# Kernel optimization log

Measured on AMD Instinct MI355X. Metric: run time of the kernel, lower is better.

The kernel has to match this reference:

```python
import jax, jax.numpy as jnp
import numpy as np

EMB_DIM = 2048
N_HEADS = 32
N_KV_HEADS = 8
HEAD_DIM = EMB_DIM // N_HEADS  # 64
N_REP = N_HEADS // N_KV_HEADS  # 4
B = 1
T = 2048


def setup_inputs() -> dict:
    key = jax.random.key(0)
    ks = jax.random.split(key, 7)
    x = jax.random.normal(ks[0], (B, T, EMB_DIM), dtype=jnp.float32)
    # RoPE tables, standard: cos/sin of shape (T, head_dim)
    inv_freq = 1.0 / (10000.0 ** (np.arange(0, HEAD_DIM, 2, dtype=np.float32) / HEAD_DIM))
    pos = np.arange(T, dtype=np.float32)
    ang = pos[:, None] * inv_freq[None, :]            # (T, head_dim/2)
    ang = np.concatenate([ang, ang], axis=-1)         # (T, head_dim)
    cos = jnp.asarray(np.cos(ang), dtype=jnp.float32)
    sin = jnp.asarray(np.sin(ang), dtype=jnp.float32)
    s = 0.02
    Wq = jax.random.normal(ks[1], (EMB_DIM, EMB_DIM), dtype=jnp.float32) * s
    Wk = jax.random.normal(ks[2], (N_KV_HEADS * HEAD_DIM, EMB_DIM), dtype=jnp.float32) * s
    Wv = jax.random.normal(ks[3], (N_KV_HEADS * HEAD_DIM, EMB_DIM), dtype=jnp.float32) * s
    Wo = jax.random.normal(ks[4], (EMB_DIM, EMB_DIM), dtype=jnp.float32) * s
    return {"x": x, "cos": cos, "sin": sin, "Wq": Wq, "Wk": Wk, "Wv": Wv, "Wo": Wo}


def apply_rope(t, cos, sin):
    # t: (b, h, T, d); cos/sin: (T, d)
    d = t.shape[-1]
    x1, x2 = t[..., : d // 2], t[..., d // 2:]
    rotated = jnp.concatenate([-x2, x1], axis=-1)
    return t * cos[None, None] + rotated * sin[None, None]


def reference(x, cos, sin, Wq, Wk, Wv, Wo):
    b, n_tok, _ = x.shape
    q = (x @ Wq.T).reshape(b, n_tok, N_HEADS, HEAD_DIM).transpose(0, 2, 1, 3)
    k = (x @ Wk.T).reshape(b, n_tok, N_KV_HEADS, HEAD_DIM).transpose(0, 2, 1, 3)
    v = (x @ Wv.T).reshape(b, n_tok, N_KV_HEADS, HEAD_DIM).transpose(0, 2, 1, 3)
    q = apply_rope(q, cos, sin)
    k = apply_rope(k, cos, sin)
    # repeat_interleave KV heads to n_heads
    k = jnp.repeat(k, N_REP, axis=1)
    v = jnp.repeat(v, N_REP, axis=1)
    scores = jnp.einsum("bhqd,bhkd->bhqk", q, k) / jnp.sqrt(jnp.float32(HEAD_DIM))
    causal = jnp.tril(jnp.ones((n_tok, n_tok), dtype=bool))
    scores = jnp.where(causal[None, None], scores, -jnp.inf)
    weights = jax.nn.softmax(scores, axis=-1)
    ctx = jnp.einsum("bhqk,bhkd->bhqd", weights, v)
    ctx = ctx.transpose(0, 2, 1, 3).reshape(b, n_tok, EMB_DIM)
    return ctx @ Wo.T
```

## Files before the change

kernel.cpp:

```cpp
#include <hip/hip_runtime.h>
#include <hip/hip_bf16.h>
#include <stdint.h>

#define EMB   2048
#define TOK   2048
#define NH    32
#define NKV   8
#define HD    64
#define QKVN  3072

typedef __attribute__((ext_vector_type(8))) short bf16x8;
typedef __attribute__((ext_vector_type(4))) float f32x4;
typedef __attribute__((ext_vector_type(16))) float f32x16;
typedef __attribute__((ext_vector_type(4))) unsigned int u32x4;

__device__ __forceinline__ void gld16(const void* g, void* l) {
  auto gp = reinterpret_cast<const int __attribute__((address_space(1)))*>(
      reinterpret_cast<uintptr_t>(g));
  auto lp = reinterpret_cast<int __attribute__((address_space(3)))*>(
      reinterpret_cast<uintptr_t>(l));
  __builtin_amdgcn_global_load_lds(gp, lp, 16, 0, 0);
}

__device__ __forceinline__ unsigned int cvtpk_bf16(float lo, float hi) {
  unsigned int r;
  asm("v_cvt_pk_bf16_f32 %0, %1, %2" : "=v"(r) : "v"(lo), "v"(hi));
  return r;
}
__device__ __forceinline__ void pl32swap(unsigned int &a, unsigned int &b) {
  asm volatile("v_permlane32_swap_b32 %0, %1" : "+v"(a), "+v"(b));
}
__device__ __forceinline__ float fexp2(float x) {
  float r;
  asm("v_exp_f32 %0, %1" : "=v"(r) : "v"(x));
  return r;
}

__global__ void cast_all(const float* __restrict__ x,  const float* __restrict__ wq,
                         const float* __restrict__ wk, const float* __restrict__ wv,
                         const float* __restrict__ wo,
                         __hip_bfloat16* __restrict__ xb,
                         __hip_bfloat16* __restrict__ wc,
                         __hip_bfloat16* __restrict__ wob) {
  const size_t M4 = (size_t)4 * 1024 * 1024;
  const size_t M1 = (size_t)1024 * 1024;
  size_t i = ((size_t)blockIdx.x * 256 + threadIdx.x) * 4;
  const float* src;
  __hip_bfloat16* dst;
  if (i < M4)                    { src = x  + i;                 dst = xb  + i; }
  else if (i < 2*M4)             { src = wq + (i - M4);          dst = wc  + (i - M4); }
  else if (i < 2*M4 + M1)        { src = wk + (i - 2*M4);        dst = wc  + M4 + (i - 2*M4); }
  else if (i < 2*M4 + 2*M1)      { src = wv + (i - 2*M4 - M1);   dst = wc  + M4 + M1 + (i - 2*M4 - M1); }
  else                           { src = wo + (i - 2*M4 - 2*M1); dst = wob + (i - 2*M4 - 2*M1); }
  float4 v = *reinterpret_cast<const float4*>(src);
  dst[0] = __float2bfloat16(v.x);
  dst[1] = __float2bfloat16(v.y);
  dst[2] = __float2bfloat16(v.z);
  dst[3] = __float2bfloat16(v.w);
}

template<int BN, typename OT>
__global__ __launch_bounds__(512) void gemm8(const __hip_bfloat16* __restrict__ A,
                                             const __hip_bfloat16* __restrict__ B,
                                             OT* __restrict__ C,
                                             int M, int N, int K) {
  constexpr int A_BYTES = 128 * 128;
  constexpr int B_BYTES = BN * 128;
  constexpr int SLOT    = A_BYTES + B_BYTES;
  constexpr int CA = 2;
  constexpr int CB = BN / 64;
  constexpr int NR = BN / 64;
  extern __shared__ char lds[];

  const int nbc = N / BN;
  const int nwg = gridDim.x;
  int bid = blockIdx.x;
  bid = (bid & 7) * (nwg >> 3) + (bid >> 3);
  const int br = bid / nbc, bc = bid % nbc;

  const int tid  = threadIdx.x;
  const int w    = tid >> 6;
  const int lane = tid & 63;
  const int wr   = w >> 2, wc = w & 3;
  const int l15  = lane & 15, lg = lane >> 4;
  const int axor = (l15 & 7) << 4;

  const __hip_bfloat16* Ag = A + (size_t)br * 128 * K;
  const __hip_bfloat16* Bg = B + (size_t)bc * BN * K;

  const int srow = lane >> 3;
  const int scol = (((lane & 7) ^ srow) << 3);

  auto stageA = [&](char* slot, int kt) {
#pragma unroll
    for (int i = 0; i < CA; ++i) {
      const int c = w * CA + i;
      gld16(Ag + (size_t)(c * 8 + srow) * K + kt + scol, slot + c * 1024);
    }
  };
  auto stageB = [&](char* slot, int kt) {
#pragma unroll
    for (int i = 0; i < CB; ++i) {
      const int c = w * CB + i;
      gld16(Bg + (size_t)(c * 8 + srow) * K + kt + scol, slot + A_BYTES + c * 1024);
    }
  };
  auto ldA = [&](const char* sa, int m, int kk) {
    return *reinterpret_cast<const bf16x8*>(
        sa + (wr * 64 + m * 16 + l15) * 128 + ((kk * 64 + lg * 16) ^ axor));
  };
  auto ldB = [&](const char* sa, int n, int kk) {
    return *reinterpret_cast<const bf16x8*>(
        sa + A_BYTES + (wc * (BN / 4) + n * 16 + l15) * 128 + ((kk * 64 + lg * 16) ^ axor));
  };

  f32x4 acc[4][NR];
#pragma unroll
  for (int m = 0; m < 4; ++m)
#pragma unroll
    for (int n = 0; n < NR; ++n) acc[m][n] = (f32x4){0.f, 0.f, 0.f, 0.f};

  const int nt = K >> 6;

  stageA(lds, 0);         stageB(lds, 0);
  stageA(lds + SLOT, 64); stageB(lds + SLOT, 64);
  if constexpr (CA + CB == 4) asm volatile("s_waitcnt vmcnt(4)" ::: "memory");
  else                        asm volatile("s_waitcnt vmcnt(5)" ::: "memory");
  __builtin_amdgcn_s_barrier();

  int slc = 0, sls = 2;
  for (int t = 0; t < nt; ++t) {
    const char* sa = lds + slc * SLOT;
    char* stg = lds + sls * SLOT;
    const bool do_stage = (t + 2) < nt;
    const int kt2 = (t + 2) << 6;

    bf16x8 afr[2][2], bfr[NR][2];
#pragma unroll
    for (int m = 0; m < 2; ++m)
#pragma unroll
      for (int kk = 0; kk < 2; ++kk) afr[m][kk] = ldA(sa, m, kk);
#pragma unroll
    for (int n = 0; n < NR; ++n)
#pragma unroll
      for (int kk = 0; kk < 2; ++kk) bfr[n][kk] = ldB(sa, n, kk);
    if (do_stage) stageA(stg, kt2);
    __builtin_amdgcn_s_barrier();
    asm volatile("s_waitcnt lgkmcnt(0)" ::: "memory");
    __builtin_amdgcn_sched_barrier(0);
    __builtin_amdgcn_s_setprio(1);
#pragma unroll
    for (int m = 0; m < 2; ++m)
#pragma unroll
      for (int n = 0; n < NR; ++n)
#pragma unroll
        for (int kk = 0; kk < 2; ++kk)
          acc[m][n] = __builtin_amdgcn_mfma_f32_16x16x32_bf16(afr[m][kk], bfr[n][kk],
                                                              acc[m][n], 0, 0, 0);
    __builtin_amdgcn_s_setprio(0);
    __builtin_amdgcn_s_barrier();

#pragma unroll
    for (int m = 0; m < 2; ++m)
#pragma unroll
      for (int kk = 0; kk < 2; ++kk) afr[m][kk] = ldA(sa, 2 + m, kk);
    if (do_stage) stageB(stg, kt2);
    __builtin_amdgcn_s_barrier();
    asm volatile("s_waitcnt lgkmcnt(0)" ::: "memory");
    __builtin_amdgcn_sched_barrier(0);
    __builtin_amdgcn_s_setprio(1);
#pragma unroll
    for (int m = 0; m < 2; ++m)
#pragma unroll
      for (int n = 0; n < NR; ++n)
#pragma unroll
        for (int kk = 0; kk < 2; ++kk)
          acc[2 + m][n] = __builtin_amdgcn_mfma_f32_16x16x32_bf16(afr[m][kk], bfr[n][kk],
                                                                  acc[2 + m][n], 0, 0, 0);
    __builtin_amdgcn_s_setprio(0);
    if (t < nt - 2) {
      if constexpr (CA + CB == 4) asm volatile("s_waitcnt vmcnt(4)" ::: "memory");
      else                        asm volatile("s_waitcnt vmcnt(5)" ::: "memory");
    } else {
      asm volatile("s_waitcnt vmcnt(0)" ::: "memory");
    }
    __builtin_amdgcn_s_barrier();

    slc = (slc == 2) ? 0 : slc + 1;
    sls = (sls == 2) ? 0 : sls + 1;
  }

  const int row0 = br * 128 + wr * 64;
  const int col0 = bc * BN + wc * (BN / 4);
#pragma unroll
  for (int m = 0; m < 4; ++m)
#pragma unroll
    for (int n = 0; n < NR; ++n)
#pragma unroll
      for (int r = 0; r < 4; ++r) {
        const size_t off = (size_t)(row0 + m * 16 + lg * 4 + r) * N + col0 + n * 16 + l15;
        if constexpr (sizeof(OT) == 4) C[off] = acc[m][n][r];
        else                           C[off] = __float2bfloat16(acc[m][n][r]);
      }
}

#define QSCALE 0.1803368801111243f

__device__ __forceinline__ size_t kq_idx(int tile_row, int t, int d) {
  return ((size_t)tile_row) * 2048 +
         ((((d >> 4) * 64) + (((d >> 3) & 1) * 32) + (t & 31)) << 3) + (d & 7);
}

__global__ void rope_cast(const __hip_bfloat16* __restrict__ qkv,
                          const float* __restrict__ cosT, const float* __restrict__ sinT,
                          __hip_bfloat16* __restrict__ Qf,
                          __hip_bfloat16* __restrict__ Kf,
                          __hip_bfloat16* __restrict__ Vf) {
  const int QP = TOK * NH * (HD / 2);
  const int KP = TOK * NKV * (HD / 2);
  int idx = blockIdx.x * 256 + threadIdx.x;
  if (idx < QP) {
    int d = idx & 31, h = (idx >> 5) & 31, t = idx >> 10;
    const __hip_bfloat16* row = qkv + (size_t)t * QKVN + h * 64;
    float x1 = __bfloat162float(row[d]), x2 = __bfloat162float(row[d + 32]);
    float o1 = (x1 * cosT[t * 64 + d]      - x2 * sinT[t * 64 + d])      * QSCALE;
    float o2 = (x2 * cosT[t * 64 + d + 32] + x1 * sinT[t * 64 + d + 32]) * QSCALE;
    const int tile_row = h * 64 + (t >> 5);
    Qf[kq_idx(tile_row, t, d)]      = __float2bfloat16(o1);
    Qf[kq_idx(tile_row, t, d + 32)] = __float2bfloat16(o2);
  } else if (idx < QP + KP) {
    int j = idx - QP;
    int d = j & 31, hk = (j >> 5) & 7, t = j >> 8;
    const __hip_bfloat16* row = qkv + (size_t)t * QKVN + 2048 + hk * 64;
    float x1 = __bfloat162float(row[d]), x2 = __bfloat162float(row[d + 32]);
    float o1 = x1 * cosT[t * 64 + d]      - x2 * sinT[t * 64 + d];
    float o2 = x2 * cosT[t * 64 + d + 32] + x1 * sinT[t * 64 + d + 32];
    const int tile_row = hk * 64 + (t >> 5);
    Kf[kq_idx(tile_row, t, d)]      = __float2bfloat16(o1);
    Kf[kq_idx(tile_row, t, d + 32)] = __float2bfloat16(o2);
  } else {
    int vj = idx - QP - KP;
    int d = vj & 63, t = (vj >> 6) & (TOK - 1), hk = vj >> 17;
    const __hip_bfloat16 v = qkv[(size_t)t * QKVN + 2560 + hk * 64 + d];
    const size_t tb = ((size_t)hk * 64 + (t >> 5)) * 2048;
    const int c = (((t >> 4) & 1) * 128) + ((d >> 5) * 64) + (((t >> 3) & 1) * 32) + (d & 31);
    Vf[tb + (c << 3) + (t & 7)] = v;
  }
}

#define MBIAS 10.0f
#define PART_BYTES (8 * 32 * 33 * 4)
#define SMEM_BYTES (PART_BYTES + 8 * 2 * 32 * 4)

__global__ __launch_bounds__(512, 4) void attnL(const __hip_bfloat16* __restrict__ Qf,
                                                const __hip_bfloat16* __restrict__ Kf,
                                                const __hip_bfloat16* __restrict__ Vf,
                                                __hip_bfloat16* __restrict__ ctx) {
  const int idx   = blockIdx.x;
  const int hk    = idx & 7;
  const int strip = 63 - (idx >> 3);
  const int tid   = threadIdx.x;
  const int w     = tid >> 6;
  const int lane  = tid & 63;
  const int l31   = lane & 31, hi = lane >> 5;
  const int hq    = w & 3;
  const int pr    = w >> 2;
  const int h     = hk * 4 + hq;
  const int q0    = strip * 32;
  const int niter = (strip >> 1) + 1;

  __shared__ char smem[SMEM_BYTES];
  auto part_u = reinterpret_cast<unsigned int(*)[32][33]>(smem);
  auto mlb    = reinterpret_cast<float(*)[2][32]>(smem + PART_BYTES);

  const __hip_bfloat16* Kt = Kf + (size_t)hk * 64 * 2048;
  const __hip_bfloat16* Vt = Vf + (size_t)hk * 64 * 2048;

  const __hip_bfloat16* Qp = Qf + ((size_t)h * 64 + strip) * 2048 + lane * 8;
  bf16x8 qf[4];
#pragma unroll
  for (int ks = 0; ks < 4; ++ks)
    qf[ks] = *reinterpret_cast<const bf16x8*>(Qp + ks * 512);

  f32x16 minit;
#pragma unroll
  for (int r = 0; r < 16; ++r) minit[r] = -MBIAS;

  f32x16 oa0, oa1;
#pragma unroll
  for (int r = 0; r < 16; ++r) { oa0[r] = 0.f; oa1[r] = 0.f; }
  float mb = 0.f, l = 0.f;

  const int sseg = w >> 1, shh = w & 1;
  const __hip_bfloat16* sbase = (sseg < 2) ? Kt : Vt;
  auto stage_pair = [&](int buf, int it) {
    const int tt = 2 * it + (sseg & 1);
    const int tc = (tt <= strip) ? tt : strip;
    const __hip_bfloat16* src = sbase + (size_t)tc * 2048 + shh * 1024 + lane * 8;
    char* dst = &smem[buf * 16384 + ((sseg >= 2) ? 8192 : 0) + (sseg & 1) * 4096 + shh * 2048];
    gld16(src,       dst);
    gld16(src + 512, dst + 1024);
  };

  stage_pair(0, 0);
  __syncthreads();

  for (int it = 0; it < niter; ++it) {
    if (it + 1 < niter) stage_pair((it + 1) & 1, it + 1);

    const int t = 2 * it + pr;
    if (t <= strip) {
      const char* kb = &smem[(it & 1) * 16384 + pr * 4096];
      const char* vb = &smem[(it & 1) * 16384 + 8192 + pr * 4096];
      const int lo = lane * 16;
      const bf16x8 k0 = *reinterpret_cast<const bf16x8*>(kb + lo);
      const bf16x8 k1 = *reinterpret_cast<const bf16x8*>(kb + 1024 + lo);
      const bf16x8 k2 = *reinterpret_cast<const bf16x8*>(kb + 2048 + lo);
      const bf16x8 k3 = *reinterpret_cast<const bf16x8*>(kb + 3072 + lo);

      __builtin_amdgcn_s_setprio(1);
      f32x16 st = __builtin_amdgcn_mfma_f32_32x32x16_bf16(k0, qf[0], minit, 0, 0, 0);
      st = __builtin_amdgcn_mfma_f32_32x32x16_bf16(k1, qf[1], st, 0, 0, 0);
      st = __builtin_amdgcn_mfma_f32_32x32x16_bf16(k2, qf[2], st, 0, 0, 0);
      st = __builtin_amdgcn_mfma_f32_32x32x16_bf16(k3, qf[3], st, 0, 0, 0);
      __builtin_amdgcn_s_setprio(0);

      float s[16];
#pragma unroll
      for (int r = 0; r < 16; ++r) s[r] = st[r];
      if (t == strip) {
#pragma unroll
        for (int r = 0; r < 16; ++r) {
          const int crow = (r & 3) + 8 * (r >> 2) + 4 * hi;
          s[r] = (crow <= l31) ? s[r] : -1e30f;
        }
      }
      float a0 = fmaxf(fmaxf(s[0], s[1]),  s[2]);
      float a1 = fmaxf(fmaxf(s[3], s[4]),  s[5]);
      float a2 = fmaxf(fmaxf(s[6], s[7]),  s[8]);
      float a3 = fmaxf(fmaxf(s[9], s[10]), s[11]);
      float a4 = fmaxf(fmaxf(s[12], s[13]), s[14]);
      float rmax = fmaxf(fmaxf(fmaxf(fmaxf(a0, a1), a2), fmaxf(a3, a4)), s[15]);
      rmax = fmaxf(rmax, __shfl_xor(rmax, 32));

      if (!__all(rmax <= mb + 8.0f)) {
        const float mnew = fmaxf(mb, rmax);
        const float resc = fexp2(mb - mnew);
        l *= resc;
#pragma unroll
        for (int r = 0; r < 16; ++r) { oa0[r] *= resc; oa1[r] *= resc; }
        mb = mnew;
      }

      float p[16];
      if (mb == 0.0f) {
#pragma unroll
        for (int r = 0; r < 16; ++r) p[r] = fexp2(s[r]);
      } else {
#pragma unroll
        for (int r = 0; r < 16; ++r) p[r] = fexp2(s[r] - mb);
      }
      float u0 = (p[0] + p[1]) + (p[2] + p[3]);
      float u1 = (p[4] + p[5]) + (p[6] + p[7]);
      float u2 = (p[8] + p[9]) + (p[10] + p[11]);
      float u3 = (p[12] + p[13]) + (p[14] + p[15]);
      float rsum = (u0 + u1) + (u2 + u3);
      rsum += __shfl_xor(rsum, 32);
      l += rsum;

      unsigned int wpk[8];
#pragma unroll
      for (int j = 0; j < 8; ++j) wpk[j] = cvtpk_bf16(p[2 * j], p[2 * j + 1]);

      const bf16x8 v00 = *reinterpret_cast<const bf16x8*>(vb + lo);
      const bf16x8 v10 = *reinterpret_cast<const bf16x8*>(vb + 1024 + lo);
      const bf16x8 v01 = *reinterpret_cast<const bf16x8*>(vb + 2048 + lo);
      const bf16x8 v11 = *reinterpret_cast<const bf16x8*>(vb + 3072 + lo);

      __builtin_amdgcn_s_setprio(1);
      {
        unsigned int x0 = wpk[0], y0 = wpk[2];  pl32swap(x0, y0);
        unsigned int x1 = wpk[1], y1 = wpk[3];  pl32swap(x1, y1);
        u32x4 pw; pw[0] = x0; pw[1] = x1; pw[2] = y0; pw[3] = y1;
        bf16x8 pf = *reinterpret_cast<bf16x8*>(&pw);
        oa0 = __builtin_amdgcn_mfma_f32_32x32x16_bf16(v00, pf, oa0, 0, 0, 0);
        oa1 = __builtin_amdgcn_mfma_f32_32x32x16_bf16(v10, pf, oa1, 0, 0, 0);
      }
      {
        unsigned int x0 = wpk[4], y0 = wpk[6];  pl32swap(x0, y0);
        unsigned int x1 = wpk[5], y1 = wpk[7];  pl32swap(x1, y1);
        u32x4 pw; pw[0] = x0; pw[1] = x1; pw[2] = y0; pw[3] = y1;
        bf16x8 pf = *reinterpret_cast<bf16x8*>(&pw);
        oa0 = __builtin_amdgcn_mfma_f32_32x32x16_bf16(v01, pf, oa0, 0, 0, 0);
        oa1 = __builtin_amdgcn_mfma_f32_32x32x16_bf16(v11, pf, oa1, 0, 0, 0);
      }
      __builtin_amdgcn_s_setprio(0);
    }
    __syncthreads();
  }

#pragma unroll
  for (int r = 0; r < 16; ++r) {
    const int d0 = (r & 3) + 8 * (r >> 2) + 4 * hi;
    part_u[w][d0][l31] = cvtpk_bf16(oa0[r], oa1[r]);
  }
  if (hi == 0) { mlb[w][0][l31] = mb; mlb[w][1][l31] = l; }
  __syncthreads();

  const int d  = tid & 63;
  const int g  = tid >> 6;
  const int mh = g & 3, qh = g >> 2;
  const int w0 = mh, w1 = mh + 4;
#pragma unroll
  for (int qq = 0; qq < 16; ++qq) {
    const int q = qh * 16 + qq;
    const float m0 = mlb[w0][0][q], m1 = mlb[w1][0][q];
    const float M = fmaxf(m0, m1);
    const float s0 = fexp2(m0 - M), s1 = fexp2(m1 - M);
    const float L = mlb[w0][1][q] * s0 + mlb[w1][1][q] * s1;
    const unsigned int u0 = part_u[w0][d & 31][q];
    const unsigned int u1 = part_u[w1][d & 31][q];
    const unsigned int b0 = (d < 32) ? (u0 << 16) : (u0 & 0xffff0000u);
    const unsigned int b1 = (d < 32) ? (u1 << 16) : (u1 & 0xffff0000u);
    const float p0 = __uint_as_float(b0), p1 = __uint_as_float(b1);
    ctx[(size_t)(q0 + q) * EMB + (hk * 4 + mh) * HD + d] =
        __float2bfloat16((p0 * s0 + p1 * s1) / L);
  }
}

extern "C" void kernel_launch(void* const* d_in, const int* in_sizes, int n_in,
                              void* d_out, int out_size, void* d_ws, size_t ws_size,
                              hipStream_t stream) {
  const float* x    = (const float*)d_in[0];
  const float* cosT = (const float*)d_in[1];
  const float* sinT = (const float*)d_in[2];
  const float* Wq   = (const float*)d_in[3];
  const float* Wk   = (const float*)d_in[4];
  const float* Wv   = (const float*)d_in[5];
  const float* Wo   = (const float*)d_in[6];
  float* out = (float*)d_out;

  const size_t M4 = (size_t)4 * 1024 * 1024;
  const size_t M1 = (size_t)1024 * 1024;

  char* ws = (char*)d_ws;
  __hip_bfloat16* xb   = (__hip_bfloat16*)ws;
  __hip_bfloat16* Wc   = xb + M4;
  __hip_bfloat16* Wob  = Wc + (size_t)6 * M1;
  __hip_bfloat16* qkvb = Wob + M4;
  __hip_bfloat16* Qf   = qkvb + (size_t)TOK * QKVN;
  __hip_bfloat16* Kf   = Qf + (size_t)NH * TOK * HD;
  __hip_bfloat16* Vf   = Kf + (size_t)NKV * TOK * HD;
  __hip_bfloat16* ctxb = Vf + (size_t)NKV * HD * TOK;

  constexpr int SLOT192 = 128 * 128 + 192 * 128;
  constexpr int SLOT128 = 128 * 128 + 128 * 128;
  hipFuncSetAttribute(reinterpret_cast<const void*>(&gemm8<192, __hip_bfloat16>),
                      hipFuncAttributeMaxDynamicSharedMemorySize, 3 * SLOT192);
  hipFuncSetAttribute(reinterpret_cast<const void*>(&gemm8<128, float>),
                      hipFuncAttributeMaxDynamicSharedMemorySize, 3 * SLOT128);

  cast_all<<<14336, 256, 0, stream>>>(x, Wq, Wk, Wv, Wo, xb, Wc, Wob);

  gemm8<192, __hip_bfloat16><<<256, 512, 3 * SLOT192, stream>>>(xb, Wc, qkvb,
                                                                TOK, QKVN, EMB);

  rope_cast<<<14336, 256, 0, stream>>>(qkvb, cosT, sinT, Qf, Kf, Vf);

  attnL<<<64 * 8, 512, 0, stream>>>(Qf, Kf, Vf, ctxb);

  gemm8<128, float><<<256, 512, 3 * SLOT128, stream>>>(ctxb, Wob, out, TOK, EMB, EMB);
}
```

Measured before the change: 119.1 us.

## Split attention KV range into two chunks with a separate merge kernel

Each query strip's causal KV loop is split into two halves handled by separate blocks, doubling the grid from 512 to 1024 blocks. Each block writes unnormalized partial outputs plus max and sum stats to workspace, and a new merge kernel combines the two partials and normalizes. The aim is better load balance and occupancy for the triangular causal workload. The cost is an extra launch, extra global traffic for the partials, and partials stored in bf16 before normalization. The partial buffers reuse the start of the workspace, overlapping the xb/Wc region, which is safe only because those buffers are dead by then.

```diff
diff --git a/kernel.cpp b/kernel.cpp
--- a/kernel.cpp
+++ b/kernel.cpp
@@ -252,13 +252,16 @@
 #define PART_BYTES (8 * 32 * 33 * 4)
 #define SMEM_BYTES (PART_BYTES + 8 * 2 * 32 * 4)
 
-__global__ __launch_bounds__(512, 4) void attnL(const __hip_bfloat16* __restrict__ Qf,
+__global__ __launch_bounds__(512, 4) void attnS(const __hip_bfloat16* __restrict__ Qf,
                                                 const __hip_bfloat16* __restrict__ Kf,
                                                 const __hip_bfloat16* __restrict__ Vf,
-                                                __hip_bfloat16* __restrict__ ctx) {
+                                                __hip_bfloat16* __restrict__ po16,
+                                                float* __restrict__ pml) {
   const int idx   = blockIdx.x;
   const int hk    = idx & 7;
-  const int strip = 63 - (idx >> 3);
+  const int c     = (idx >> 3) & 1;
+  const int strip = 63 - (idx >> 4);
+  const int chunkIdx = idx >> 3;
   const int tid   = threadIdx.x;
   const int w     = tid >> 6;
   const int lane  = tid & 63;
@@ -266,8 +269,11 @@
   const int hq    = w & 3;
   const int pr    = w >> 2;
   const int h     = hk * 4 + hq;
-  const int q0    = strip * 32;
-  const int niter = (strip >> 1) + 1;
+
+  const int nitT = (strip >> 1) + 1;
+  const int len0 = (nitT + 1) >> 1;
+  const int it0  = c ? len0 : 0;
+  const int itN  = c ? (nitT - len0) : len0;
 
   __shared__ char smem[SMEM_BYTES];
   auto part_u = reinterpret_cast<unsigned int(*)[32][33]>(smem);
@@ -302,100 +308,105 @@
     gld16(src + 512, dst + 1024);
   };
 
-  stage_pair(0, 0);
-  __syncthreads();
-
-  for (int it = 0; it < niter; ++it) {
-    if (it + 1 < niter) stage_pair((it + 1) & 1, it + 1);
-
-    const int t = 2 * it + pr;
-    if (t <= strip) {
-      const char* kb = &smem[(it & 1) * 16384 + pr * 4096];
-      const char* vb = &smem[(it & 1) * 16384 + 8192 + pr * 4096];
-      const int lo = lane * 16;
-      const bf16x8 k0 = *reinterpret_cast<const bf16x8*>(kb + lo);
-      const bf16x8 k1 = *reinterpret_cast<const bf16x8*>(kb + 1024 + lo);
-      const bf16x8 k2 = *reinterpret_cast<const bf16x8*>(kb + 2048 + lo);
-      const bf16x8 k3 = *reinterpret_cast<const bf16x8*>(kb + 3072 + lo);
-
-      __builtin_amdgcn_s_setprio(1);
-      f32x16 st = __builtin_amdgcn_mfma_f32_32x32x16_bf16(k0, qf[0], minit, 0, 0, 0);
-      st = __builtin_amdgcn_mfma_f32_32x32x16_bf16(k1, qf[1], st, 0, 0, 0);
-      st = __builtin_amdgcn_mfma_f32_32x32x16_bf16(k2, qf[2], st, 0, 0, 0);
-      st = __builtin_amdgcn_mfma_f32_32x32x16_bf16(k3, qf[3], st, 0, 0, 0);
-      __builtin_amdgcn_s_setprio(0);
-
-      float s[16];
-#pragma unroll
-      for (int r = 0; r < 16; ++r) s[r] = st[r];
-      if (t == strip) {
-#pragma unroll
-        for (int r = 0; r < 16; ++r) {
-          const int crow = (r & 3) + 8 * (r >> 2) + 4 * hi;
-          s[r] = (crow <= l31) ? s[r] : -1e30f;
+  if (itN > 0) {
+    stage_pair(0, it0);
+    __syncthreads();
+
+    for (int k = 0; k < itN; ++k) {
+      const int it = it0 + k;
+      if (k + 1 < itN) stage_pair((k + 1) & 1, it + 1);
+
+      const int t = 2 * it + pr;
+      if (t <= strip) {
+        const char* kb = &smem[(k & 1) * 16384 + pr * 4096];
+        const char* vb = &smem[(k & 1) * 16384 + 8192 + pr * 4096];
+        const int lo = lane * 16;
+        const bf16x8 k0 = *reinterpret_cast<const bf16x8*>(kb + lo);
+        const bf16x8 k1 = *reinterpret_cast<const bf16x8*>(kb + 1024 + lo);
+        const bf16x8 k2 = *reinterpret_cast<const bf16x8*>(kb + 2048 + lo);
+        const bf16x8 k3 = *reinterpret_cast<const bf16x8*>(kb + 3072 + lo);
+
+        __builtin_amdgcn_s_setprio(1);
+        f32x16 st = __builtin_amdgcn_mfma_f32_32x32x16_bf16(k0, qf[0], minit, 0, 0, 0);
+        st = __builtin_amdgcn_mfma_f32_32x32x16_bf16(k1, qf[1], st, 0, 0, 0);
+        st = __builtin_amdgcn_mfma_f32_32x32x16_bf16(k2, qf[2], st, 0, 0, 0);
+        st = __builtin_amdgcn_mfma_f32_32x32x16_bf16(k3, qf[3], st, 0, 0, 0);
+        __builtin_amdgcn_s_setprio(0);
+
+        float s[16];
+#pragma unroll
+        for (int r = 0; r < 16; ++r) s[r] = st[r];
+        if (t == strip) {
+#pragma unroll
+          for (int r = 0; r < 16; ++r) {
+            const int crow = (r & 3) + 8 * (r >> 2) + 4 * hi;
+            s[r] = (crow <= l31) ? s[r] : -1e30f;
+          }
         }
+        float a0 = fmaxf(fmaxf(s[0], s[1]),  s[2]);
+        float a1 = fmaxf(fmaxf(s[3], s[4]),  s[5]);
+        float a2 = fmaxf(fmaxf(s[6], s[7]),  s[8]);
+        float a3 = fmaxf(fmaxf(s[9], s[10]), s[11]);
+        float a4 = fmaxf(fmaxf(s[12], s[13]), s[14]);
+        float rmax = fmaxf(fmaxf(fmaxf(fmaxf(a0, a1), a2), fmaxf(a3, a4)), s[15]);
+        rmax = fmaxf(rmax, __shfl_xor(rmax, 32));
+
+        if (!__all(rmax <= mb + 8.0f)) {
+          const float mnew = fmaxf(mb, rmax);
+          const float resc = fexp2(mb - mnew);
+          l *= resc;
+#pragma unroll
+          for (int r = 0; r < 16; ++r) { oa0[r] *= resc; oa1[r] *= resc; }
+          mb = mnew;
+        }
+
+        float p[16];
+        if (mb == 0.0f) {
+#pragma unroll
+          for (int r = 0; r < 16; ++r) p[r] = fexp2(s[r]);
+        } else {
+#pragma unroll
+          for (int r = 0; r < 16; ++r) p[r] = fexp2(s[r] - mb);
+        }
+        float u0 = (p[0] + p[1]) + (p[2] + p[3]);
+        float u1 = (p[4] + p[5]) + (p[6] + p[7]);
+        float u2 = (p[8] + p[9]) + (p[10] + p[11]);
+        float u3 = (p[12] + p[13]) + (p[14] + p[15]);
+        float rsum = (u0 + u1) + (u2 + u3);
+        rsum += __shfl_xor(rsum, 32);
+        l += rsum;
+
+        unsigned int wpk[8];
+#pragma unroll
+        for (int j = 0; j < 8; ++j) wpk[j] = cvtpk_bf16(p[2 * j], p[2 * j + 1]);
+
+        const bf16x8 v00 = *reinterpret_cast<const bf16x8*>(vb + lo);
+        const bf16x8 v10 = *reinterpret_cast<const bf16x8*>(vb + 1024 + lo);
+        const bf16x8 v01 = *reinterpret_cast<const bf16x8*>(vb + 2048 + lo);
+        const bf16x8 v11 = *reinterpret_cast<const bf16x8*>(vb + 3072 + lo);
+
+        __builtin_amdgcn_s_setprio(1);
+        {
+          unsigned int x0 = wpk[0], y0 = wpk[2];  pl32swap(x0, y0);
+          unsigned int x1 = wpk[1], y1 = wpk[3];  pl32swap(x1, y1);
+          u32x4 pw; pw[0] = x0; pw[1] = x1; pw[2] = y0; pw[3] = y1;
+          bf16x8 pf = *reinterpret_cast<bf16x8*>(&pw);
+          oa0 = __builtin_amdgcn_mfma_f32_32x32x16_bf16(v00, pf, oa0, 0, 0, 0);
+          oa1 = __builtin_amdgcn_mfma_f32_32x32x16_bf16(v10, pf, oa1, 0, 0, 0);
+        }
+        {
+          unsigned int x0 = wpk[4], y0 = wpk[6];  pl32swap(x0, y0);
+          unsigned int x1 = wpk[5], y1 = wpk[7];  pl32swap(x1, y1);
+          u32x4 pw; pw[0] = x0; pw[1] = x1; pw[2] = y0; pw[3] = y1;
+          bf16x8 pf = *reinterpret_cast<bf16x8*>(&pw);
+          oa0 = __builtin_amdgcn_mfma_f32_32x32x16_bf16(v01, pf, oa0, 0, 0, 0);
+          oa1 = __builtin_amdgcn_mfma_f32_32x32x16_bf16(v11, pf, oa1, 0, 0, 0);
+        }
+        __builtin_amdgcn_s_setprio(0);
       }
-      float a0 = fmaxf(fmaxf(s[0], s[1]),  s[2]);
-      float a1 = fmaxf(fmaxf(s[3], s[4]),  s[5]);
-      float a2 = fmaxf(fmaxf(s[6], s[7]),  s[8]);
-      float a3 = fmaxf(fmaxf(s[9], s[10]), s[11]);
-      float a4 = fmaxf(fmaxf(s[12], s[13]), s[14]);
-      float rmax = fmaxf(fmaxf(fmaxf(fmaxf(a0, a1), a2), fmaxf(a3, a4)), s[15]);
-      rmax = fmaxf(rmax, __shfl_xor(rmax, 32));
-
-      if (!__all(rmax <= mb + 8.0f)) {
-        const float mnew = fmaxf(mb, rmax);
-        const float resc = fexp2(mb - mnew);
-        l *= resc;
-#pragma unroll
-        for (int r = 0; r < 16; ++r) { oa0[r] *= resc; oa1[r] *= resc; }
-        mb = mnew;
-      }
-
-      float p[16];
-      if (mb == 0.0f) {
-#pragma unroll
-        for (int r = 0; r < 16; ++r) p[r] = fexp2(s[r]);
-      } else {
-#pragma unroll
-        for (int r = 0; r < 16; ++r) p[r] = fexp2(s[r] - mb);
-      }
-      float u0 = (p[0] + p[1]) + (p[2] + p[3]);
-      float u1 = (p[4] + p[5]) + (p[6] + p[7]);
-      float u2 = (p[8] + p[9]) + (p[10] + p[11]);
-      float u3 = (p[12] + p[13]) + (p[14] + p[15]);
-      float rsum = (u0 + u1) + (u2 + u3);
-      rsum += __shfl_xor(rsum, 32);
-      l += rsum;
-
-      unsigned int wpk[8];
-#pragma unroll
-      for (int j = 0; j < 8; ++j) wpk[j] = cvtpk_bf16(p[2 * j], p[2 * j + 1]);
-
-      const bf16x8 v00 = *reinterpret_cast<const bf16x8*>(vb + lo);
-      const bf16x8 v10 = *reinterpret_cast<const bf16x8*>(vb + 1024 + lo);
-      const bf16x8 v01 = *reinterpret_cast<const bf16x8*>(vb + 2048 + lo);
-      const bf16x8 v11 = *reinterpret_cast<const bf16x8*>(vb + 3072 + lo);
-
-      __builtin_amdgcn_s_setprio(1);
-      {
-        unsigned int x0 = wpk[0], y0 = wpk[2];  pl32swap(x0, y0);
-        unsigned int x1 = wpk[1], y1 = wpk[3];  pl32swap(x1, y1);
-        u32x4 pw; pw[0] = x0; pw[1] = x1; pw[2] = y0; pw[3] = y1;
-        bf16x8 pf = *reinterpret_cast<bf16x8*>(&pw);
-        oa0 = __builtin_amdgcn_mfma_f32_32x32x16_bf16(v00, pf, oa0, 0, 0, 0);
-        oa1 = __builtin_amdgcn_mfma_f32_32x32x16_bf16(v10, pf, oa1, 0, 0, 0);
-      }
-      {
-        unsigned int x0 = wpk[4], y0 = wpk[6];  pl32swap(x0, y0);
-        unsigned int x1 = wpk[5], y1 = wpk[7];  pl32swap(x1, y1);
-        u32x4 pw; pw[0] = x0; pw[1] = x1; pw[2] = y0; pw[3] = y1;
-        bf16x8 pf = *reinterpret_cast<bf16x8*>(&pw);
-        oa0 = __builtin_amdgcn_mfma_f32_32x32x16_bf16(v01, pf, oa0, 0, 0, 0);
-        oa1 = __builtin_amdgcn_mfma_f32_32x32x16_bf16(v11, pf, oa1, 0, 0, 0);
-      }
-      __builtin_amdgcn_s_setprio(0);
+      __syncthreads();
     }
+  } else {
     __syncthreads();
   }
 
@@ -411,6 +422,7 @@
   const int g  = tid >> 6;
   const int mh = g & 3, qh = g >> 2;
   const int w0 = mh, w1 = mh + 4;
+  const int slot = chunkIdx * 32 + hk * 4 + mh;
 #pragma unroll
   for (int qq = 0; qq < 16; ++qq) {
     const int q = qh * 16 + qq;
@@ -423,8 +435,34 @@
     const unsigned int b0 = (d < 32) ? (u0 << 16) : (u0 & 0xffff0000u);
     const unsigned int b1 = (d < 32) ? (u1 << 16) : (u1 & 0xffff0000u);
     const float p0 = __uint_as_float(b0), p1 = __uint_as_float(b1);
-    ctx[(size_t)(q0 + q) * EMB + (hk * 4 + mh) * HD + d] =
-        __float2bfloat16((p0 * s0 + p1 * s1) / L);
+    po16[(size_t)slot * 2048 + q * 64 + d] = __float2bfloat16(p0 * s0 + p1 * s1);
+    if (d == 0) { pml[slot * 64 + q] = M; pml[slot * 64 + 32 + q] = L; }
+  }
+}
+
+__global__ __launch_bounds__(256) void attn_m2(const __hip_bfloat16* __restrict__ po16,
+                                               const float* __restrict__ pml,
+                                               __hip_bfloat16* __restrict__ ctx) {
+  const int b  = blockIdx.x;
+  const int h  = b & 31;
+  const int sp = b >> 5;
+  const int strip = 63 - sp;
+  const int s0 = (sp * 2 + 0) * 32 + h;
+  const int s1 = (sp * 2 + 1) * 32 + h;
+  const int q0 = strip * 32;
+  const int tid = threadIdx.x;
+#pragma unroll
+  for (int p = 0; p < 8; ++p) {
+    const int e = p * 256 + tid;
+    const int q = e >> 6, d = e & 63;
+    const float m0 = pml[s0 * 64 + q], l0 = pml[s0 * 64 + 32 + q];
+    const float m1 = pml[s1 * 64 + q], l1 = pml[s1 * 64 + 32 + q];
+    const float M  = fmaxf(m0, m1);
+    const float c0 = fexp2(m0 - M), c1 = fexp2(m1 - M);
+    const float L  = l0 * c0 + l1 * c1;
+    const float v  = __bfloat162float(po16[(size_t)s0 * 2048 + e]) * c0 +
+                     __bfloat162float(po16[(size_t)s1 * 2048 + e]) * c1;
+    ctx[(size_t)(q0 + q) * EMB + h * HD + d] = __float2bfloat16(v / L);
   }
 }
 
@@ -453,6 +491,9 @@
   __hip_bfloat16* Vf   = Kf + (size_t)NKV * TOK * HD;
   __hip_bfloat16* ctxb = Vf + (size_t)NKV * HD * TOK;
 
+  __hip_bfloat16* po16 = (__hip_bfloat16*)ws;
+  float*          pml  = (float*)(ws + (size_t)16 * 1024 * 1024);
+
   constexpr int SLOT192 = 128 * 128 + 192 * 128;
   constexpr int SLOT128 = 128 * 128 + 128 * 128;
   hipFuncSetAttribute(reinterpret_cast<const void*>(&gemm8<192, __hip_bfloat16>),
@@ -467,7 +508,8 @@
 
   rope_cast<<<14336, 256, 0, stream>>>(qkvb, cosT, sinT, Qf, Kf, Vf);
 
-  attnL<<<64 * 8, 512, 0, stream>>>(Qf, Kf, Vf, ctxb);
+  attnS<<<1024, 512, 0, stream>>>(Qf, Kf, Vf, po16, pml);
+  attn_m2<<<2048, 256, 0, stream>>>(po16, pml, ctxb);
 
   gemm8<128, float><<<256, 512, 3 * SLOT128, stream>>>(ctxb, Wob, out, TOK, EMB, EMB);
 }
```

Measured after the change: 124.5 us. 1.05x slower.
